# Kernel tuning notes

Measured on AMD Instinct MI355X. Metric: run time of the kernel, lower is better.

The kernel has to match this reference:

```python
import jax, jax.numpy as jnp
import numpy as np

H, W = 32, 64          # img_size
NB = 4                 # fno_blocks
SCALE = 0.02


def setup_inputs() -> dict:
    key = jax.random.key(0)
    ks = jax.random.split(key, 8)
    B, N, C = 16, H * W, 768
    BS = C // NB
    x = jax.random.normal(ks[0], (B, N, C), dtype=jnp.float32)
    w1 = SCALE * jax.random.normal(ks[1], (2, NB, BS, BS), dtype=jnp.float32)
    b1 = SCALE * jax.random.normal(ks[2], (2, NB, BS), dtype=jnp.float32)
    w2 = SCALE * jax.random.normal(ks[3], (2, NB, BS, BS), dtype=jnp.float32)
    b2 = SCALE * jax.random.normal(ks[4], (2, NB, BS), dtype=jnp.float32)
    # Conv1d(C, C, kernel_size=1) == per-token linear layer over channels
    bias_w = jax.random.normal(ks[5], (C, C), dtype=jnp.float32) / np.sqrt(C)
    bias_b = jax.random.normal(ks[6], (C,), dtype=jnp.float32) * 0.01
    return {"x": x, "w1": w1, "b1": b1, "w2": w2, "b2": b2,
            "bias_w": bias_w, "bias_b": bias_b}


def _mul(a, w):
    # block-diagonal matmul: a [..., NB, BS], w [NB, BS, BS]
    return jnp.einsum('...bd,bdk->...bk', a, w)


def reference(x, w1, b1, w2, b2, bias_w, bias_b):
    B, N, C = x.shape
    BS = C // NB
    # Conv1d kernel-size-1 bias path
    bias = x @ bias_w.T + bias_b
    # spatial FFT
    xf = jnp.fft.rfftn(x.reshape(B, H, W, C), axes=(1, 2), norm='ortho')
    xf = xf.reshape(B, H, W // 2 + 1, NB, BS)
    xr, xi = xf.real, xf.imag
    # layer 1 (complex block-diag matmul + bias, ReLU on real/imag separately)
    r1 = jax.nn.relu(_mul(xr, w1[0]) - _mul(xi, w1[1]) + b1[0])
    i1 = jax.nn.relu(_mul(xr, w1[1]) + _mul(xi, w1[0]) + b1[1])
    # layer 2 -- NOTE: imag part uses the *updated* real part, matching the
    # original torch code's in-place reassignment order.
    r2 = _mul(r1, w2[0]) - _mul(i1, w2[1]) + b2[0]
    i2 = _mul(r2, w2[1]) + _mul(i1, w2[0]) + b2[1]
    xc = jax.lax.complex(r2, i2).reshape(B, H, W // 2 + 1, C)
    out = jnp.fft.irfftn(xc, s=(H, W), axes=(1, 2), norm='ortho')
    return out.reshape(B, N, C) + bias
```

## Files before the change

kernel.cpp:

```cpp
#include <hip/hip_runtime.h>
#include <hip/hip_bf16.h>
#include <stdint.h>

#define BB 16
#define HH 32
#define WW 64
#define CC 768
#define W2C 33
#define ROWW (2*CC)

typedef __bf16 bf16x8 __attribute__((ext_vector_type(8)));
typedef float f32x4 __attribute__((ext_vector_type(4)));

__device__ __forceinline__ unsigned short f2bf(float f) {
  __hip_bfloat16 h = __float2bfloat16(f);
  return __builtin_bit_cast(unsigned short, h);
}
__device__ __forceinline__ float bf2f(unsigned short u) {
  union { unsigned int i; float f; } x;
  x.i = ((unsigned int)u) << 16;
  return x.f;
}

__device__ __forceinline__ void g2l16(const void* g, void* l) {
  __builtin_amdgcn_global_load_lds((const __attribute__((address_space(1))) unsigned int*)g,
                                   (__attribute__((address_space(3))) unsigned int*)l,
                                   16, 0, 0);
}

__device__ __host__ constexpr int brevc(int x, int bits) {
  int r = 0;
  for (int i = 0; i < bits; ++i) r |= ((x >> i) & 1) << (bits - 1 - i);
  return r;
}

template<int N, bool INV>
__device__ __forceinline__ void fft_reg(float2 (&v)[N], const float2* __restrict__ tw) {
  constexpr int LOG2N = (N == 64) ? 6 : 5;
#pragma unroll
  for (int s = 0; s < LOG2N; ++s) {
    const int len = N >> s;
    const int half = len >> 1;
    const int tstep = 64 / len;
#pragma unroll
    for (int i = 0; i < N; i += len) {
#pragma unroll
      for (int j = 0; j < half; ++j) {
        float2 u = v[i + j];
        float2 t = v[i + j + half];
        float sr = u.x + t.x, si = u.y + t.y;
        float dr = u.x - t.x, di = u.y - t.y;
        float2 w = tw[j * tstep];
        float wr = w.x;
        float wi = INV ? -w.y : w.y;
        v[i + j] = make_float2(sr, si);
        v[i + j + half] = make_float2(dr * wr - di * wi, dr * wi + di * wr);
      }
    }
  }
}

#define TW_INIT()                                                            \
  __shared__ float2 tw[64];                                                  \
  if (threadIdx.x < 64) {                                                    \
    float ang = (float)threadIdx.x * 0.09817477042468103f;       \
    tw[threadIdx.x] = make_float2(cosf(ang), -sinf(ang));                    \
  }                                                                          \
  __syncthreads();

__global__ __launch_bounds__(256) void fft_fwd_w(const float* __restrict__ x,
                                                 ushort2* __restrict__ yw,
                                                 unsigned short* __restrict__ xb) {
  __shared__ float2 tw[64];
  __shared__ __align__(16) float xs[32][256];
  const int t = threadIdx.x;
  if (t < 64) {
    float ang = (float)t * 0.09817477042468103f;
    tw[t] = make_float2(cosf(ang), -sinf(ang));
  }
  const int bh = blockIdx.x;
  const int c0 = blockIdx.y * 256;
  const float* xrow = x + (size_t)bh * (WW * CC) + c0;
  unsigned short* xbrow = xb + (size_t)bh * (WW * CC) + c0;
  const int rg = t >> 6;
  const int lc = (t & 63) * 4;
  float2 v[32];
#pragma unroll
  for (int half = 0; half < 2; ++half) {
    __syncthreads();
#pragma unroll
    for (int it = 0; it < 8; ++it) {
      const int w = half * 32 + it * 4 + rg;
      float4 f = *(const float4*)(xrow + (size_t)w * CC + lc);
      *(float4*)&xs[it * 4 + rg][lc] = f;
      *(ushort4*)(xbrow + (size_t)w * CC + lc) =
          make_ushort4(f2bf(f.x), f2bf(f.y), f2bf(f.z), f2bf(f.w));
    }
    __syncthreads();
#pragma unroll
    for (int n = 0; n < 16; ++n)
      v[half * 16 + n] = make_float2(xs[2 * n][t], xs[2 * n + 1][t]);
  }
  fft_reg<32, false>(v, tw);
  ushort2* yp = yw + (size_t)bh * (W2C * CC) + c0 + t;
  {
    float2 Z0 = v[0];
    yp[0] = make_ushort2(f2bf(Z0.x + Z0.y), f2bf(0.f));
    yp[(size_t)32 * CC] = make_ushort2(f2bf(Z0.x - Z0.y), f2bf(0.f));
  }
#pragma unroll
  for (int k = 1; k < 32; ++k) {
    float2 Zk = v[brevc(k, 5)];
    float2 Zm = v[brevc(32 - k, 5)];
    float Er = 0.5f * (Zk.x + Zm.x), Ei = 0.5f * (Zk.y - Zm.y);
    float Odr = 0.5f * (Zk.y + Zm.y), Odi = -0.5f * (Zk.x - Zm.x);
    float2 w = tw[k];
    float Xr = Er + w.x * Odr - w.y * Odi;
    float Xi = Ei + w.x * Odi + w.y * Odr;
    yp[(size_t)k * CC] = make_ushort2(f2bf(Xr), f2bf(Xi));
  }
}

__global__ __launch_bounds__(256) void fft_fwd_h(const ushort2* __restrict__ yw,
                                                 unsigned short* __restrict__ xf) {
  TW_INIT();
  const int bk = blockIdx.x;
  const int b = bk / W2C, kw = bk - b * W2C;
  const int c = blockIdx.y * 256 + threadIdx.x;
  const ushort2* yp = yw + ((size_t)b * HH * W2C + kw) * CC + c;
  float2 v[32];
#pragma unroll
  for (int h = 0; h < 32; ++h) {
    ushort2 u = yp[(size_t)h * (W2C * CC)];
    v[h] = make_float2(bf2f(u.x), bf2f(u.y));
  }
  fft_reg<32, false>(v, tw);
  const int nb = c / 192, cc = c - nb * 192;
  unsigned short* xp = xf + (size_t)nb * 384 + cc;
  const float s = 0.022097086912079608f;
#pragma unroll
  for (int kh = 0; kh < 32; ++kh) {
    float2 z = v[brevc(kh, 5)];
    size_t m = ((size_t)b * HH + kh) * W2C + kw;
    xp[m * ROWW] = f2bf(z.x * s);
    xp[m * ROWW + 192] = f2bf(z.y * s);
  }
}

__global__ __launch_bounds__(256) void fft_inv_h(const unsigned short* __restrict__ r2,
                                                 ushort2* __restrict__ g) {
  TW_INIT();
  const int bk = blockIdx.x;
  const int b = bk / W2C, kw = bk - b * W2C;
  const int c = blockIdx.y * 256 + threadIdx.x;
  const int nb = c / 192, cc = c - nb * 192;
  const unsigned short* rp = r2 + (size_t)nb * 384 + cc;
  float2 v[32];
#pragma unroll
  for (int kh = 0; kh < 32; ++kh) {
    size_t m = ((size_t)b * HH + kh) * W2C + kw;
    v[kh] = make_float2(bf2f(rp[m * ROWW]), bf2f(rp[m * ROWW + 192]));
  }
  fft_reg<32, true>(v, tw);
  ushort2* gp = g + ((size_t)b * HH * W2C + kw) * CC + c;
#pragma unroll
  for (int h = 0; h < 32; ++h) {
    float2 z = v[brevc(h, 5)];
    gp[(size_t)h * (W2C * CC)] = make_ushort2(f2bf(z.x), f2bf(z.y));
  }
}

__global__ __launch_bounds__(256) void fft_inv_w(const ushort2* __restrict__ g,
                                                 const unsigned short* __restrict__ biasb,
                                                 float* __restrict__ out) {
  __shared__ float2 tw[64];
  __shared__ __align__(16) float ys[32][256];
  const int t = threadIdx.x;
  if (t < 64) {
    float ang = (float)t * 0.09817477042468103f;
    tw[t] = make_float2(cosf(ang), -sinf(ang));
  }
  __syncthreads();
  const int bh = blockIdx.x;
  const int c0 = blockIdx.y * 256;
  const ushort2* gp = g + (size_t)bh * (W2C * CC) + c0 + t;
  float2 v[32];
  {
    float X0 = bf2f(gp[0].x);
    float X32 = bf2f(gp[(size_t)32 * CC].x);
    v[0] = make_float2(0.5f * (X0 + X32), 0.5f * (X0 - X32));
  }
#pragma unroll
  for (int k = 1; k < 32; ++k) {
    ushort2 uk = gp[(size_t)k * CC];
    ushort2 um = gp[(size_t)(32 - k) * CC];
    float2 Xk = make_float2(bf2f(uk.x), bf2f(uk.y));
    float2 Xm = make_float2(bf2f(um.x), bf2f(um.y));
    float Ar = 0.5f * (Xk.x + Xm.x), Ai = 0.5f * (Xk.y - Xm.y);
    float Dr = 0.5f * (Xk.x - Xm.x), Di = 0.5f * (Xk.y + Xm.y);
    float2 w = tw[k];
    float Br = w.x * Dr + w.y * Di;
    float Bi = w.x * Di - w.y * Dr;
    v[k] = make_float2(Ar - Bi, Ai + Br);
  }
  fft_reg<32, true>(v, tw);
  const float s2 = 0.04419417382415922f;
  float* orow = out + (size_t)bh * (WW * CC) + c0;
  const unsigned short* brow = biasb + (size_t)bh * (WW * CC) + c0;
  const int rg = t >> 6;
  const int lc = (t & 63) * 4;
#pragma unroll
  for (int half = 0; half < 2; ++half) {
    __syncthreads();
#pragma unroll
    for (int n = 0; n < 16; ++n) {
      float2 z = v[brevc(half * 16 + n, 5)];
      ys[2 * n][t] = z.x * s2;
      ys[2 * n + 1][t] = z.y * s2;
    }
    __syncthreads();
#pragma unroll
    for (int it = 0; it < 8; ++it) {
      const int w = half * 32 + it * 4 + rg;
      float4 f = *(const float4*)&ys[it * 4 + rg][lc];
      ushort4 b4 = *(const ushort4*)(brow + (size_t)w * CC + lc);
      f.x += bf2f(b4.x); f.y += bf2f(b4.y); f.z += bf2f(b4.z); f.w += bf2f(b4.w);
      *(float4*)(orow + (size_t)w * CC + lc) = f;
    }
  }
}

template<bool RELU, bool OBF>
__global__ __launch_bounds__(256) void gemm_bt(
    const unsigned short* __restrict__ A, int lda, int aZ,
    const unsigned short* __restrict__ Bw, int K, int bZ,
    const float* __restrict__ bias, int biasZ,
    void* __restrict__ outp, int ldo, int oZ) {
  __shared__ __align__(16) unsigned short As[128 * 32];
  __shared__ __align__(16) unsigned short Bs[128 * 32];
  const int t = threadIdx.x;
  const int z = blockIdx.z;
  const size_t m0 = (size_t)blockIdx.x * 128;
  const int n0 = blockIdx.y * 128;
  const unsigned short* Ap = A + m0 * lda + (size_t)z * aZ;
  const unsigned short* Bp = Bw + (size_t)n0 * K + (size_t)z * bZ;
  const int lane = t & 63, wave = t >> 6;
  const int lr = lane & 15, quad = lane >> 4;
  const int wm = (wave >> 1) * 64, wn = (wave & 1) * 64;
  const int row = t >> 2;
  const int sl = t & 3;
  const int kb = (sl ^ ((row >> 1) & 3)) * 8;
  const int swzf = (lr >> 1) & 3;
  f32x4 acc[4][4] = {};
  for (int k0 = 0; k0 < K; k0 += 32) {
    const unsigned short* ga = Ap + (size_t)row * lda + (k0 + kb);
    g2l16(ga, &As[row * 32 + sl * 8]);
    g2l16(ga + (size_t)64 * lda, &As[(row + 64) * 32 + sl * 8]);
    const unsigned short* gb = Bp + (size_t)row * K + (k0 + kb);
    g2l16(gb, &Bs[row * 32 + sl * 8]);
    g2l16(gb + (size_t)64 * K, &Bs[(row + 64) * 32 + sl * 8]);
    __syncthreads();
    bf16x8 af[4], bfr[4];
#pragma unroll
    for (int mi = 0; mi < 4; ++mi)
      af[mi] = *(const bf16x8*)&As[(wm + mi * 16 + lr) * 32 + ((quad ^ swzf) * 8)];
#pragma unroll
    for (int ni = 0; ni < 4; ++ni)
      bfr[ni] = *(const bf16x8*)&Bs[(wn + ni * 16 + lr) * 32 + ((quad ^ swzf) * 8)];
#pragma unroll
    for (int mi = 0; mi < 4; ++mi)
#pragma unroll
      for (int ni = 0; ni < 4; ++ni)
        acc[mi][ni] = __builtin_amdgcn_mfma_f32_16x16x32_bf16(af[mi], bfr[ni], acc[mi][ni], 0, 0, 0);
    __syncthreads();
  }
#pragma unroll
  for (int mi = 0; mi < 4; ++mi) {
    const size_t mrow = m0 + wm + mi * 16 + quad * 4;
#pragma unroll
    for (int ni = 0; ni < 4; ++ni) {
      const int ncol = n0 + wn + ni * 16 + lr;
      const float bv = bias[z * biasZ + ncol];
#pragma unroll
      for (int r = 0; r < 4; ++r) {
        float vv = acc[mi][ni][r] + bv;
        if (RELU) vv = fmaxf(vv, 0.f);
        const size_t off = (mrow + r) * (size_t)ldo + (size_t)z * oZ + ncol;
        if (OBF) ((unsigned short*)outp)[off] = f2bf(vv);
        else ((float*)outp)[off] = vv;
      }
    }
  }
}

__global__ __launch_bounds__(256) void cvt_bf16(const float* __restrict__ in,
                                                unsigned short* __restrict__ outp) {
  const size_t i = ((size_t)blockIdx.x * 256 + threadIdx.x) * 4;
  float4 v = *(const float4*)(in + i);
  ushort4 o = make_ushort4(f2bf(v.x), f2bf(v.y), f2bf(v.z), f2bf(v.w));
  *(ushort4*)(outp + i) = o;
}

__global__ __launch_bounds__(256) void build_w1(const float* __restrict__ w1,
                                                const float* __restrict__ b1,
                                                unsigned short* __restrict__ w1t,
                                                float* __restrict__ bias1) {
  const int idx = blockIdx.x * 256 + threadIdx.x;
  const int nb = idx / (384 * 384);
  const int rem = idx - nb * (384 * 384);
  const int n = rem / 384, k = rem - (rem / 384) * 384;
  const bool khi = k >= 192, nhi = n >= 192;
  const int kk = khi ? k - 192 : k, nn = nhi ? n - 192 : n;
  float val;
  if (!khi && !nhi)      val =  w1[((0 * 4 + nb) * 192 + kk) * 192 + nn];
  else if (khi && !nhi)  val = -w1[((1 * 4 + nb) * 192 + kk) * 192 + nn];
  else if (!khi && nhi)  val =  w1[((1 * 4 + nb) * 192 + kk) * 192 + nn];
  else                   val =  w1[((0 * 4 + nb) * 192 + kk) * 192 + nn];
  w1t[((size_t)nb * 384 + n) * 384 + k] = f2bf(val);
  if (k == 0)
    bias1[nb * 384 + n] = nhi ? b1[(1 * 4 + nb) * 192 + nn] : b1[(0 * 4 + nb) * 192 + nn];
}

__global__ __launch_bounds__(256) void build_w2(const float* __restrict__ w2,
                                                const float* __restrict__ b2,
                                                unsigned short* __restrict__ w2t,
                                                float* __restrict__ bias2) {
  const int idx = blockIdx.x * 256 + threadIdx.x;
  const int nb = idx / (384 * 384);
  const int rem = idx - nb * (384 * 384);
  const int n = rem / 384, k = rem - (rem / 384) * 384;
  const bool khi = k >= 192, nhi = n >= 192;
  const int kk = khi ? k - 192 : k, nn = nhi ? n - 192 : n;
  float val;
  if (!khi && !nhi) {
    val = w2[((0 * 4 + nb) * 192 + kk) * 192 + nn];
  } else if (khi && !nhi) {
    val = -w2[((1 * 4 + nb) * 192 + kk) * 192 + nn];
  } else if (!khi && nhi) {
    float s = 0.f;
    for (int d = 0; d < 192; ++d)
      s += w2[((0 * 4 + nb) * 192 + kk) * 192 + d] * w2[((1 * 4 + nb) * 192 + d) * 192 + nn];
    val = s;
  } else {
    float s = 0.f;
    for (int d = 0; d < 192; ++d)
      s += w2[((1 * 4 + nb) * 192 + kk) * 192 + d] * w2[((1 * 4 + nb) * 192 + d) * 192 + nn];
    val = w2[((0 * 4 + nb) * 192 + kk) * 192 + nn] - s;
  }
  w2t[((size_t)nb * 384 + n) * 384 + k] = f2bf(val);
  if (k == 0) {
    float bv;
    if (!nhi) {
      bv = b2[(0 * 4 + nb) * 192 + nn];
    } else {
      float s = 0.f;
      for (int d = 0; d < 192; ++d)
        s += b2[(0 * 4 + nb) * 192 + d] * w2[((1 * 4 + nb) * 192 + d) * 192 + nn];
      bv = b2[(1 * 4 + nb) * 192 + nn] + s;
    }
    bias2[nb * 384 + n] = bv;
  }
}

extern "C" void kernel_launch(void* const* d_in, const int* in_sizes, int n_in,
                              void* d_out, int out_size, void* d_ws, size_t ws_size,
                              hipStream_t stream) {
  (void)in_sizes; (void)n_in; (void)out_size; (void)ws_size;
  const float* x  = (const float*)d_in[0];
  const float* w1 = (const float*)d_in[1];
  const float* b1 = (const float*)d_in[2];
  const float* w2 = (const float*)d_in[3];
  const float* b2 = (const float*)d_in[4];
  const float* bw = (const float*)d_in[5];
  const float* bb = (const float*)d_in[6];
  float* out = (float*)d_out;

  char* p = (char*)d_ws;
  unsigned short* buf1 = (unsigned short*)p; p += 51904512;
  unsigned short* buf2 = (unsigned short*)p; p += 51904512;
  unsigned short* buf3 = (unsigned short*)p; p += 51904512;
  unsigned short* bwb  = (unsigned short*)p; p += 1179648;
  unsigned short* w1t  = (unsigned short*)p; p += 1179648;
  unsigned short* w2t  = (unsigned short*)p; p += 1179648;
  float* bias1 = (float*)p; p += 6144;
  float* bias2 = (float*)p; p += 6144;

  cvt_bf16<<<589824 / 1024, 256, 0, stream>>>(bw, bwb);
  build_w1<<<589824 / 256, 256, 0, stream>>>(w1, b1, w1t, bias1);
  build_w2<<<589824 / 256, 256, 0, stream>>>(w2, b2, w2t, bias2);
  fft_fwd_w<<<dim3(BB * HH, 3), 256, 0, stream>>>(x, (ushort2*)buf1, buf2);
  fft_fwd_h<<<dim3(BB * W2C, 3), 256, 0, stream>>>((const ushort2*)buf1, buf3);
  gemm_bt<true, true><<<dim3(132, 3, 4), 256, 0, stream>>>(
      buf3, ROWW, 384, w1t, 384, 384 * 384, bias1, 384, buf1, ROWW, 384);
  gemm_bt<false, true><<<dim3(256, 6, 1), 256, 0, stream>>>(
      buf2, 768, 0, bwb, 768, 0, bb, 0, buf3, 768, 0);
  gemm_bt<false, true><<<dim3(132, 3, 4), 256, 0, stream>>>(
      buf1, ROWW, 384, w2t, 384, 384 * 384, bias2, 384, buf2, ROWW, 384);
  fft_inv_h<<<dim3(BB * W2C, 3), 256, 0, stream>>>(buf2, (ushort2*)buf1);
  fft_inv_w<<<dim3(BB * HH, 3), 256, 0, stream>>>((const ushort2*)buf1, buf3, out);
}
```

Measured before the change: 468.5 us.

## Use compile-time twiddles and drop LDS transposes in W-axis FFT kernels

Twiddle factors become compile-time constants built with constexpr Taylor series, which removes the shared-memory twiddle table, its sin/cos setup and a barrier in every FFT kernel. The W-direction forward and inverse kernels also drop their LDS staging transpose. Each thread now reads and writes its own channel column directly, using scalar loads strided by C. This cuts shared memory and synchronisation, but replaces float4 and ushort4 vector accesses with scalar 4-byte and 2-byte per-lane accesses, which may coalesce less efficiently.

```diff
diff --git a/kernel.cpp b/kernel.cpp
--- a/kernel.cpp
+++ b/kernel.cpp
@@ -34,8 +34,38 @@
   return r;
 }
 
+constexpr double TPI = 6.283185307179586476925286766559;
+constexpr double tsin_(double x) {
+  double t = x, s = x, x2 = x * x;
+  for (int i = 1; i < 14; ++i) { t *= -x2 / (double)((2 * i) * (2 * i + 1)); s += t; }
+  return s;
+}
+constexpr double tcos_(double x) {
+  double t = 1.0, s = 1.0, x2 = x * x;
+  for (int i = 1; i < 14; ++i) { t *= -x2 / (double)((2 * i - 1) * (2 * i)); s += t; }
+  return s;
+}
+struct Tw64 { float c[64]; float s[64]; };
+constexpr Tw64 mk_tw() {
+  Tw64 r{};
+  for (int k = 0; k < 64; ++k) {
+    int q = k >> 4, m = k & 15;
+    double a = (TPI / 64.0) * m;
+    double cq = tcos_(a), sq = tsin_(a);
+    double c, s;
+    if (q == 0)      { c =  cq; s =  sq; }
+    else if (q == 1) { c = -sq; s =  cq; }
+    else if (q == 2) { c = -cq; s = -sq; }
+    else             { c =  sq; s = -cq; }
+    r.c[k] = (float)c;
+    r.s[k] = (float)(-s);
+  }
+  return r;
+}
+constexpr Tw64 TW = mk_tw();
+
 template<int N, bool INV>
-__device__ __forceinline__ void fft_reg(float2 (&v)[N], const float2* __restrict__ tw) {
+__device__ __forceinline__ void fft_reg(float2 (&v)[N]) {
   constexpr int LOG2N = (N == 64) ? 6 : 5;
 #pragma unroll
   for (int s = 0; s < LOG2N; ++s) {
@@ -50,9 +80,8 @@
         float2 t = v[i + j + half];
         float sr = u.x + t.x, si = u.y + t.y;
         float dr = u.x - t.x, di = u.y - t.y;
-        float2 w = tw[j * tstep];
-        float wr = w.x;
-        float wi = INV ? -w.y : w.y;
+        float wr = TW.c[j * tstep];
+        float wi = INV ? -TW.s[j * tstep] : TW.s[j * tstep];
         v[i + j] = make_float2(sr, si);
         v[i + j + half] = make_float2(dr * wr - di * wi, dr * wi + di * wr);
       }
@@ -60,49 +89,27 @@
   }
 }
 
-#define TW_INIT()                                                            \
-  __shared__ float2 tw[64];                                                  \
-  if (threadIdx.x < 64) {                                                    \
-    float ang = (float)threadIdx.x * 0.09817477042468103f;       \
-    tw[threadIdx.x] = make_float2(cosf(ang), -sinf(ang));                    \
-  }                                                                          \
-  __syncthreads();
-
 __global__ __launch_bounds__(256) void fft_fwd_w(const float* __restrict__ x,
                                                  ushort2* __restrict__ yw,
                                                  unsigned short* __restrict__ xb) {
-  __shared__ float2 tw[64];
-  __shared__ __align__(16) float xs[32][256];
   const int t = threadIdx.x;
-  if (t < 64) {
-    float ang = (float)t * 0.09817477042468103f;
-    tw[t] = make_float2(cosf(ang), -sinf(ang));
-  }
   const int bh = blockIdx.x;
-  const int c0 = blockIdx.y * 256;
-  const float* xrow = x + (size_t)bh * (WW * CC) + c0;
-  unsigned short* xbrow = xb + (size_t)bh * (WW * CC) + c0;
-  const int rg = t >> 6;
-  const int lc = (t & 63) * 4;
+  const int c = blockIdx.y * 256 + t;
+  const float* xp = x + (size_t)bh * (WW * CC) + c;
+  unsigned short* xbp = xb + (size_t)bh * (WW * CC) + c;
   float2 v[32];
 #pragma unroll
-  for (int half = 0; half < 2; ++half) {
-    __syncthreads();
-#pragma unroll
-    for (int it = 0; it < 8; ++it) {
-      const int w = half * 32 + it * 4 + rg;
-      float4 f = *(const float4*)(xrow + (size_t)w * CC + lc);
-      *(float4*)&xs[it * 4 + rg][lc] = f;
-      *(ushort4*)(xbrow + (size_t)w * CC + lc) =
-          make_ushort4(f2bf(f.x), f2bf(f.y), f2bf(f.z), f2bf(f.w));
-    }
-    __syncthreads();
-#pragma unroll
-    for (int n = 0; n < 16; ++n)
-      v[half * 16 + n] = make_float2(xs[2 * n][t], xs[2 * n + 1][t]);
-  }
-  fft_reg<32, false>(v, tw);
-  ushort2* yp = yw + (size_t)bh * (W2C * CC) + c0 + t;
+  for (int n = 0; n < 32; ++n) {
+    v[n].x = xp[(size_t)(2 * n) * CC];
+    v[n].y = xp[(size_t)(2 * n + 1) * CC];
+  }
+#pragma unroll
+  for (int n = 0; n < 32; ++n) {
+    xbp[(size_t)(2 * n) * CC]     = f2bf(v[n].x);
+    xbp[(size_t)(2 * n + 1) * CC] = f2bf(v[n].y);
+  }
+  fft_reg<32, false>(v);
+  ushort2* yp = yw + (size_t)bh * (W2C * CC) + c;
   {
     float2 Z0 = v[0];
     yp[0] = make_ushort2(f2bf(Z0.x + Z0.y), f2bf(0.f));
@@ -114,16 +121,15 @@
     float2 Zm = v[brevc(32 - k, 5)];
     float Er = 0.5f * (Zk.x + Zm.x), Ei = 0.5f * (Zk.y - Zm.y);
     float Odr = 0.5f * (Zk.y + Zm.y), Odi = -0.5f * (Zk.x - Zm.x);
-    float2 w = tw[k];
-    float Xr = Er + w.x * Odr - w.y * Odi;
-    float Xi = Ei + w.x * Odi + w.y * Odr;
+    float wx = TW.c[k], wy = TW.s[k];
+    float Xr = Er + wx * Odr - wy * Odi;
+    float Xi = Ei + wx * Odi + wy * Odr;
     yp[(size_t)k * CC] = make_ushort2(f2bf(Xr), f2bf(Xi));
   }
 }
 
 __global__ __launch_bounds__(256) void fft_fwd_h(const ushort2* __restrict__ yw,
                                                  unsigned short* __restrict__ xf) {
-  TW_INIT();
   const int bk = blockIdx.x;
   const int b = bk / W2C, kw = bk - b * W2C;
   const int c = blockIdx.y * 256 + threadIdx.x;
@@ -134,7 +140,7 @@
     ushort2 u = yp[(size_t)h * (W2C * CC)];
     v[h] = make_float2(bf2f(u.x), bf2f(u.y));
   }
-  fft_reg<32, false>(v, tw);
+  fft_reg<32, false>(v);
   const int nb = c / 192, cc = c - nb * 192;
   unsigned short* xp = xf + (size_t)nb * 384 + cc;
   const float s = 0.022097086912079608f;
@@ -149,7 +155,6 @@
 
 __global__ __launch_bounds__(256) void fft_inv_h(const unsigned short* __restrict__ r2,
                                                  ushort2* __restrict__ g) {
-  TW_INIT();
   const int bk = blockIdx.x;
   const int b = bk / W2C, kw = bk - b * W2C;
   const int c = blockIdx.y * 256 + threadIdx.x;
@@ -161,7 +166,7 @@
     size_t m = ((size_t)b * HH + kh) * W2C + kw;
     v[kh] = make_float2(bf2f(rp[m * ROWW]), bf2f(rp[m * ROWW + 192]));
   }
-  fft_reg<32, true>(v, tw);
+  fft_reg<32, true>(v);
   ushort2* gp = g + ((size_t)b * HH * W2C + kw) * CC + c;
 #pragma unroll
   for (int h = 0; h < 32; ++h) {
@@ -173,17 +178,10 @@
 __global__ __launch_bounds__(256) void fft_inv_w(const ushort2* __restrict__ g,
                                                  const unsigned short* __restrict__ biasb,
                                                  float* __restrict__ out) {
-  __shared__ float2 tw[64];
-  __shared__ __align__(16) float ys[32][256];
   const int t = threadIdx.x;
-  if (t < 64) {
-    float ang = (float)t * 0.09817477042468103f;
-    tw[t] = make_float2(cosf(ang), -sinf(ang));
-  }
-  __syncthreads();
   const int bh = blockIdx.x;
-  const int c0 = blockIdx.y * 256;
-  const ushort2* gp = g + (size_t)bh * (W2C * CC) + c0 + t;
+  const int c = blockIdx.y * 256 + t;
+  const ushort2* gp = g + (size_t)bh * (W2C * CC) + c;
   float2 v[32];
   {
     float X0 = bf2f(gp[0].x);
@@ -198,35 +196,20 @@
     float2 Xm = make_float2(bf2f(um.x), bf2f(um.y));
     float Ar = 0.5f * (Xk.x + Xm.x), Ai = 0.5f * (Xk.y - Xm.y);
     float Dr = 0.5f * (Xk.x - Xm.x), Di = 0.5f * (Xk.y + Xm.y);
-    float2 w = tw[k];
-    float Br = w.x * Dr + w.y * Di;
-    float Bi = w.x * Di - w.y * Dr;
+    float wx = TW.c[k], wy = TW.s[k];
+    float Br = wx * Dr + wy * Di;
+    float Bi = wx * Di - wy * Dr;
     v[k] = make_float2(Ar - Bi, Ai + Br);
   }
-  fft_reg<32, true>(v, tw);
+  fft_reg<32, true>(v);
   const float s2 = 0.04419417382415922f;
-  float* orow = out + (size_t)bh * (WW * CC) + c0;
-  const unsigned short* brow = biasb + (size_t)bh * (WW * CC) + c0;
-  const int rg = t >> 6;
-  const int lc = (t & 63) * 4;
-#pragma unroll
-  for (int half = 0; half < 2; ++half) {
-    __syncthreads();
-#pragma unroll
-    for (int n = 0; n < 16; ++n) {
-      float2 z = v[brevc(half * 16 + n, 5)];
-      ys[2 * n][t] = z.x * s2;
-      ys[2 * n + 1][t] = z.y * s2;
-    }
-    __syncthreads();
-#pragma unroll
-    for (int it = 0; it < 8; ++it) {
-      const int w = half * 32 + it * 4 + rg;
-      float4 f = *(const float4*)&ys[it * 4 + rg][lc];
-      ushort4 b4 = *(const ushort4*)(brow + (size_t)w * CC + lc);
-      f.x += bf2f(b4.x); f.y += bf2f(b4.y); f.z += bf2f(b4.z); f.w += bf2f(b4.w);
-      *(float4*)(orow + (size_t)w * CC + lc) = f;
-    }
+  float* op = out + (size_t)bh * (WW * CC) + c;
+  const unsigned short* bp = biasb + (size_t)bh * (WW * CC) + c;
+#pragma unroll
+  for (int m = 0; m < 32; ++m) {
+    float2 z = v[brevc(m, 5)];
+    op[(size_t)(2 * m) * CC]     = z.x * s2 + bf2f(bp[(size_t)(2 * m) * CC]);
+    op[(size_t)(2 * m + 1) * CC] = z.y * s2 + bf2f(bp[(size_t)(2 * m + 1) * CC]);
   }
 }
 
```

Measured after the change: 473.4 us. Within noise of the previous version (+1.0%).
